# Performance work log

Measured on AMD Instinct MI355X. Metric: run time of the kernel, lower is better.

Reference implementation:

```python
import jax, jax.numpy as jnp
import numpy as np

N_NODES = 50000
N_EDGES = 800000
IN_F = 128
HID = 128
OUT = 2


def setup_inputs() -> dict:
    key = jax.random.key(0)
    ks = jax.random.split(key, 10)
    x = jax.random.normal(ks[0], (N_NODES, IN_F), dtype=jnp.float32)
    edge_index = jax.random.randint(ks[1], (2, N_EDGES), 0, N_NODES, dtype=jnp.int64)

    def lin(k, fan_in, fan_out):
        s = 1.0 / np.sqrt(fan_in)
        return jax.random.uniform(k, (fan_in, fan_out), jnp.float32, -s, s)

    return {
        "x": x,
        "edge_index": edge_index,
        # SAGEConv1: lin_l applied to mean-aggregated neighbors (with bias),
        # lin_r applied to root features (no bias), PyG convention.
        "W1_l": lin(ks[2], IN_F, HID),
        "W1_r": lin(ks[3], IN_F, HID),
        "b1": jnp.zeros((HID,), jnp.float32),
        "W2_l": lin(ks[4], HID, HID),
        "W2_r": lin(ks[5], HID, HID),
        "b2": jnp.zeros((HID,), jnp.float32),
        "Wfc": lin(ks[6], HID, OUT),
        "bfc": jnp.zeros((OUT,), jnp.float32),
    }


def reference(x, edge_index, W1_l, W1_r, b1, W2_l, W2_r, b2, Wfc, bfc):
    n = x.shape[0]
    src = edge_index[0]  # message source j
    dst = edge_index[1]  # aggregation target i
    # in-degree for mean aggregation (clamp to avoid div-by-zero for isolated nodes)
    deg = jax.ops.segment_sum(jnp.ones_like(dst, dtype=x.dtype), dst, num_segments=n)
    inv_deg = 1.0 / jnp.maximum(deg, 1.0)  # [n]

    def sage_conv(h, Wl, Wr, b):
        # mean over incoming neighbor features, then two linear maps
        agg = jax.ops.segment_sum(h[src], dst, num_segments=n) * inv_deg[:, None]
        return agg @ Wl + h @ Wr + b

    # dropout is identity at inference (training=False)
    h = jax.nn.relu(sage_conv(x, W1_l, W1_r, b1))
    h = jax.nn.relu(sage_conv(h, W2_l, W2_r, b2))
    return h @ Wfc + bfc  # [n, out] logits
```

## Files before the change

kernel.cpp:

```cpp
#include <hip/hip_runtime.h>

#define NN 50000
#define NE 800000
#define BSHIFT 9
#define NB_BUCKET ((NN + 511) >> BSHIFT)
#define BCAP 16384
#define EPB 2048
#define NBLK_E ((NE + EPB - 1) / EPB)

#define CVT_BLKS 6250
#define PREP_BLKS 32
#define SETUP_GRID (CVT_BLKS + PREP_BLKS + 1)

typedef short short8 __attribute__((ext_vector_type(8)));
typedef short short4v __attribute__((ext_vector_type(4)));
typedef float f32x4 __attribute__((ext_vector_type(4)));
typedef _Float16 half8v __attribute__((ext_vector_type(8)));

__device__ inline unsigned short f16_bits(float f) {
    _Float16 h = (_Float16)f;
    return __builtin_bit_cast(unsigned short, h);
}

__global__ __launch_bounds__(256) void setup_kernel(const float* __restrict__ x,
                                                    unsigned short* __restrict__ xb,
                                                    const float* __restrict__ W0,
                                                    const float* __restrict__ W1,
                                                    const float* __restrict__ W2,
                                                    const float* __restrict__ W3,
                                                    short* __restrict__ wf,
                                                    int* __restrict__ cursor0) {
    int b = blockIdx.x;
    if (b < CVT_BLKS) {
        int i = b * 256 + threadIdx.x;
        float4 v = ((const float4*)x)[i];
        short4v r;
        r[0] = (short)f16_bits(v.x);
        r[1] = (short)f16_bits(v.y);
        r[2] = (short)f16_bits(v.z);
        r[3] = (short)f16_bits(v.w);
        ((short4v*)xb)[i] = r;
    } else if (b < CVT_BLKS + PREP_BLKS) {
        int t = (b - CVT_BLKS) * 256 + threadIdx.x;
        int mat = t >> 11;
        const float* W = (mat == 0) ? W0 : (mat == 1) ? W1 : (mat == 2) ? W2 : W3;
        short* out = wf + (size_t)mat * 16384;
        int r = t & 2047;
        int nt = r >> 8;
        int kc = (r >> 6) & 3;
        int lane = r & 63;
        int n = nt * 16 + (lane & 15);
        int kbase = kc * 32 + ((lane >> 4) << 3);
        short8 vh;
#pragma unroll
        for (int j = 0; j < 8; ++j) {
            float w = W[(size_t)(kbase + j) * 128 + n];
            vh[j] = (short)f16_bits(w);
        }
        size_t o = ((size_t)((nt * 4 + kc) * 64 + lane)) * 8;
        *(short8*)(out + o) = vh;
    } else {
        if (threadIdx.x < NB_BUCKET) cursor0[threadIdx.x] = 0;
    }
}

__global__ __launch_bounds__(256) void binA_kernel(const int* __restrict__ src,
                                                   const int* __restrict__ dst,
                                                   int* __restrict__ cursor0,
                                                   unsigned* __restrict__ packed, int ne) {
    __shared__ int cnt[NB_BUCKET];
    __shared__ int gstart[NB_BUCKET];
    __shared__ int cur[NB_BUCKET];
    int t = threadIdx.x;
    if (t < NB_BUCKET) cnt[t] = 0;
    __syncthreads();
    int base = blockIdx.x * EPB + t * 8;
    int s[8], d[8];
    int m = 0;
    if (base + 8 <= ne) {
        *(int4*)&s[0] = *(const int4*)(src + base);
        *(int4*)&s[4] = *(const int4*)(src + base + 4);
        *(int4*)&d[0] = *(const int4*)(dst + base);
        *(int4*)&d[4] = *(const int4*)(dst + base + 4);
        m = 8;
    } else if (base < ne) {
        m = ne - base;
        for (int i = 0; i < m; ++i) { s[i] = src[base + i]; d[i] = dst[base + i]; }
    }
    for (int i = 0; i < m; ++i) atomicAdd(&cnt[d[i] >> BSHIFT], 1);
    __syncthreads();
    if (t < NB_BUCKET) {
        gstart[t] = t * BCAP + atomicAdd(&cursor0[t], cnt[t]);
        cur[t] = 0;
    }
    __syncthreads();
    for (int i = 0; i < m; ++i) {
        int b = d[i] >> BSHIFT;
        int l = atomicAdd(&cur[b], 1);
        packed[gstart[b] + l] = ((unsigned)(d[i] & 511) << 16) | (unsigned)s[i];
    }
}

__global__ __launch_bounds__(512) void binB_kernel(const unsigned* __restrict__ packed,
                                                   const int* __restrict__ cursor0,
                                                   int* __restrict__ row_ptr,
                                                   float* __restrict__ inv_deg,
                                                   int* __restrict__ col, int n, int ne) {
    __shared__ int sdeg[512];
    __shared__ int scur[512];
    __shared__ int scnt[NB_BUCKET];
    __shared__ int sebeg[NB_BUCKET];
    int b = blockIdx.x, t = threadIdx.x;
    if (t < NB_BUCKET) scnt[t] = cursor0[t];
    sdeg[t] = 0;
    __syncthreads();
    if (t == 0) {
        int run = 0;
        for (int i = 0; i < NB_BUCKET; ++i) { sebeg[i] = run; run += scnt[i]; }
    }
    __syncthreads();
    int ebeg = sebeg[b];
    int cntE = scnt[b];
    const unsigned* pk = packed + (size_t)b * BCAP;
    for (int e = t; e < cntE; e += 512) atomicAdd(&sdeg[pk[e] >> 16], 1);
    __syncthreads();
    int v = sdeg[t];
    for (int d = 1; d < 512; d <<= 1) {
        int u = (t >= d) ? sdeg[t - d] : 0;
        __syncthreads();
        sdeg[t] += u;
        __syncthreads();
    }
    int excl = sdeg[t] - v;
    scur[t] = excl;
    int node = (b << BSHIFT) + t;
    if (node < n) {
        row_ptr[node] = ebeg + excl;
        inv_deg[node] = 1.0f / (float)(v > 0 ? v : 1);
    }
    if (b == 0 && t == 0) row_ptr[n] = ne;
    __syncthreads();
    for (int e = t; e < cntE; e += 512) {
        unsigned w = pk[e];
        int dl = w >> 16;
        int pos = ebeg + atomicAdd(&scur[dl], 1);
        col[pos] = (int)(w & 0xffffu);
    }
}

__global__ __launch_bounds__(256) void fused_sage(const unsigned short* __restrict__ hb,
                                                  const int* __restrict__ row_ptr,
                                                  const int* __restrict__ col,
                                                  const float* __restrict__ inv_deg,
                                                  const short* __restrict__ Wf0,
                                                  const short* __restrict__ Wf1,
                                                  const float* __restrict__ bias,
                                                  unsigned short* __restrict__ outb,
                                                  const float* __restrict__ Wfc,
                                                  const float* __restrict__ bfc,
                                                  float* __restrict__ fcout,
                                                  int n, int relu) {
    int lane = threadIdx.x & 63;
    int wave = threadIdx.x >> 6;
    int quad = lane >> 4, m16 = lane & 15;
    int row_base = blockIdx.x * 64 + wave * 16;
    int arow = row_base + m16;
    if (arow > n - 1) arow = n - 1;

    int beg = row_ptr[arow], end = row_ptr[arow + 1];
    float accg[4][8];
#pragma unroll
    for (int kc = 0; kc < 4; ++kc)
#pragma unroll
        for (int j = 0; j < 8; ++j) accg[kc][j] = 0.f;

    const unsigned short* tq = hb + (quad << 3);
    int e = beg;
    for (; e + 4 <= end; e += 4) {
        int c0 = col[e], c1 = col[e + 1], c2 = col[e + 2], c3 = col[e + 3];
        const unsigned short* r0 = tq + ((size_t)c0 << 7);
        const unsigned short* r1 = tq + ((size_t)c1 << 7);
        const unsigned short* r2 = tq + ((size_t)c2 << 7);
        const unsigned short* r3 = tq + ((size_t)c3 << 7);
#pragma unroll
        for (int kc = 0; kc < 4; ++kc) {
            half8v v0 = *(const half8v*)(r0 + kc * 32);
            half8v v1 = *(const half8v*)(r1 + kc * 32);
            half8v v2 = *(const half8v*)(r2 + kc * 32);
            half8v v3 = *(const half8v*)(r3 + kc * 32);
#pragma unroll
            for (int j = 0; j < 8; ++j)
                accg[kc][j] += (float)v0[j] + (float)v1[j] + ((float)v2[j] + (float)v3[j]);
        }
    }
    for (; e < end; ++e) {
        const unsigned short* r0 = tq + ((size_t)col[e] << 7);
#pragma unroll
        for (int kc = 0; kc < 4; ++kc) {
            half8v v0 = *(const half8v*)(r0 + kc * 32);
#pragma unroll
            for (int j = 0; j < 8; ++j) accg[kc][j] += (float)v0[j];
        }
    }

    float sdeg = inv_deg[arow];
    half8v a0[4];
#pragma unroll
    for (int kc = 0; kc < 4; ++kc)
#pragma unroll
        for (int j = 0; j < 8; ++j) a0[kc][j] = (_Float16)(accg[kc][j] * sdeg);

    half8v a1[4];
#pragma unroll
    for (int kc = 0; kc < 4; ++kc)
        a1[kc] = *(const half8v*)(hb + ((size_t)arow << 7) + kc * 32 + (quad << 3));

    f32x4 acc[8];
#pragma unroll
    for (int nt = 0; nt < 8; ++nt) acc[nt] = (f32x4){0.f, 0.f, 0.f, 0.f};

#pragma unroll
    for (int kc = 0; kc < 4; ++kc) {
        const short* wp0 = Wf0 + ((size_t)kc * 64 + lane) * 8;
        const short* wp1 = Wf1 + ((size_t)kc * 64 + lane) * 8;
#pragma unroll
        for (int nt = 0; nt < 8; ++nt) {
            half8v b0 = *(const half8v*)(wp0 + (size_t)nt * 2048);
            half8v b1 = *(const half8v*)(wp1 + (size_t)nt * 2048);
            acc[nt] = __builtin_amdgcn_mfma_f32_16x16x32_f16(a0[kc], b0, acc[nt], 0, 0, 0);
            acc[nt] = __builtin_amdgcn_mfma_f32_16x16x32_f16(a1[kc], b1, acc[nt], 0, 0, 0);
        }
    }

    float bcol[8];
#pragma unroll
    for (int nt = 0; nt < 8; ++nt) bcol[nt] = bias[nt * 16 + m16];

    if (Wfc) {
        float w0[8], w1[8];
#pragma unroll
        for (int nt = 0; nt < 8; ++nt) {
            float2 wv = *(const float2*)(Wfc + 2 * (nt * 16 + m16));
            w0[nt] = wv.x;
            w1[nt] = wv.y;
        }
        float b0 = bfc[0], b1 = bfc[1];
#pragma unroll
        for (int r = 0; r < 4; ++r) {
            float p0 = 0.f, p1 = 0.f;
#pragma unroll
            for (int nt = 0; nt < 8; ++nt) {
                float v = fmaxf(acc[nt][r] + bcol[nt], 0.f);
                p0 += v * w0[nt];
                p1 += v * w1[nt];
            }
#pragma unroll
            for (int off = 1; off < 16; off <<= 1) {
                p0 += __shfl_xor(p0, off, 64);
                p1 += __shfl_xor(p1, off, 64);
            }
            int row = row_base + quad * 4 + r;
            if (m16 == 0 && row < n) {
                float2 o;
                o.x = p0 + b0;
                o.y = p1 + b1;
                *(float2*)(fcout + 2 * (size_t)row) = o;
            }
        }
    } else {
#pragma unroll
        for (int r = 0; r < 4; ++r) {
            int row = row_base + quad * 4 + r;
            if (row >= n) continue;
            unsigned short* opb = outb + ((size_t)row << 7) + m16;
#pragma unroll
            for (int nt = 0; nt < 8; ++nt) {
                float v = acc[nt][r] + bcol[nt];
                if (relu) v = fmaxf(v, 0.f);
                opb[nt * 16] = f16_bits(v);
            }
        }
    }
}

extern "C" void kernel_launch(void* const* d_in, const int* in_sizes, int n_in,
                              void* d_out, int out_size, void* d_ws, size_t ws_size,
                              hipStream_t stream) {
    const float* x   = (const float*)d_in[0];
    const int* edge  = (const int*)d_in[1];
    const float* W1l = (const float*)d_in[2];
    const float* W1r = (const float*)d_in[3];
    const float* b1  = (const float*)d_in[4];
    const float* W2l = (const float*)d_in[5];
    const float* W2r = (const float*)d_in[6];
    const float* b2  = (const float*)d_in[7];
    const float* Wfc = (const float*)d_in[8];
    const float* bfc = (const float*)d_in[9];
    float* out = (float*)d_out;

    const int n = NN, ne = NE;
    const int* src = edge;
    const int* dst = edge + ne;

    char* ws = (char*)d_ws;
    size_t off = 0;
    auto alloc = [&](size_t bytes) -> char* {
        char* p = ws + off;
        off = (off + bytes + 511) & ~(size_t)511;
        return p;
    };
    int* row_ptr     = (int*)alloc((size_t)(n + 1) * 4);
    float* invdeg    = (float*)alloc((size_t)n * 4);
    int* cursor0     = (int*)alloc((size_t)NB_BUCKET * 4);
    short* wf        = (short*)alloc((size_t)4 * 16384 * 2);
    unsigned* packed = (unsigned*)alloc((size_t)NB_BUCKET * BCAP * 4);
    int* col         = (int*)alloc((size_t)ne * 4);
    unsigned short* xb   = (unsigned short*)alloc((size_t)n * 128 * 2);
    unsigned short* h1b  = (unsigned short*)alloc((size_t)n * 128 * 2);
    (void)ws_size; (void)in_sizes; (void)n_in; (void)out_size;

    setup_kernel<<<SETUP_GRID, 256, 0, stream>>>(x, xb, W1l, W1r, W2l, W2r, wf, cursor0);
    binA_kernel<<<NBLK_E, 256, 0, stream>>>(src, dst, cursor0, packed, ne);
    binB_kernel<<<NB_BUCKET, 512, 0, stream>>>(packed, cursor0, row_ptr, invdeg, col, n, ne);

    fused_sage<<<(n + 63) / 64, 256, 0, stream>>>(xb, row_ptr, col, invdeg,
                                                  wf, wf + 16384, b1, h1b,
                                                  (const float*)0, (const float*)0, (float*)0, n, 1);
    fused_sage<<<(n + 63) / 64, 256, 0, stream>>>(h1b, row_ptr, col, invdeg,
                                                  wf + 2 * 16384, wf + 3 * 16384, b2,
                                                  (unsigned short*)0, Wfc, bfc, out, n, 1);
}
```

Before: 230.5 us.

## Split neighbor gather across two waves per tile and reduce partials via LDS

Doubles the block to 512 threads so each 16-row tile gets two waves, each gathering half of every row's neighbor list, with the partial sums combined through shared memory before the MFMA stage. The gather loop is unrolled to 8 edges and sums neighbors in fp16 vector adds before converting to fp32, which cuts conversion work but loses some accumulation precision. It targets latency in the memory-bound gather by raising memory-level parallelism, at the cost of 32KB of LDS per block, a block-wide barrier, and idle upper-half waves during the matmul.

```diff
diff --git a/kernel.cpp b/kernel.cpp
--- a/kernel.cpp
+++ b/kernel.cpp
@@ -148,7 +148,7 @@
     }
 }
 
-__global__ __launch_bounds__(256) void fused_sage(const unsigned short* __restrict__ hb,
+__global__ __launch_bounds__(512) void fused_sage(const unsigned short* __restrict__ hb,
                                                   const int* __restrict__ row_ptr,
                                                   const int* __restrict__ col,
                                                   const float* __restrict__ inv_deg,
@@ -160,14 +160,28 @@
                                                   const float* __restrict__ bfc,
                                                   float* __restrict__ fcout,
                                                   int n, int relu) {
+    __shared__ float plds[32 * 256];
     int lane = threadIdx.x & 63;
-    int wave = threadIdx.x >> 6;
+    int wv = threadIdx.x >> 6;
+    int tile = wv & 3;
+    int half = wv >> 2;
     int quad = lane >> 4, m16 = lane & 15;
-    int row_base = blockIdx.x * 64 + wave * 16;
+    int row_base = blockIdx.x * 64 + tile * 16;
     int arow = row_base + m16;
     if (arow > n - 1) arow = n - 1;
 
     int beg = row_ptr[arow], end = row_ptr[arow + 1];
+    int mid = beg + ((end - beg) >> 1);
+    int gb = half ? mid : beg;
+    int ge = half ? end : mid;
+
+    half8v a1[4];
+    if (!half) {
+#pragma unroll
+        for (int kc = 0; kc < 4; ++kc)
+            a1[kc] = *(const half8v*)(hb + ((size_t)arow << 7) + kc * 32 + (quad << 3));
+    }
+
     float accg[4][8];
 #pragma unroll
     for (int kc = 0; kc < 4; ++kc)
@@ -175,33 +189,61 @@
         for (int j = 0; j < 8; ++j) accg[kc][j] = 0.f;
 
     const unsigned short* tq = hb + (quad << 3);
-    int e = beg;
-    for (; e + 4 <= end; e += 4) {
-        int c0 = col[e], c1 = col[e + 1], c2 = col[e + 2], c3 = col[e + 3];
-        const unsigned short* r0 = tq + ((size_t)c0 << 7);
-        const unsigned short* r1 = tq + ((size_t)c1 << 7);
-        const unsigned short* r2 = tq + ((size_t)c2 << 7);
-        const unsigned short* r3 = tq + ((size_t)c3 << 7);
+    int e = gb;
+    for (; e + 8 <= ge; e += 8) {
+        const unsigned short* rp[8];
+#pragma unroll
+        for (int j = 0; j < 8; ++j) rp[j] = tq + ((size_t)col[e + j] << 7);
+#pragma unroll
+        for (int kc = 0; kc < 4; ++kc) {
+            half8v v[8];
+#pragma unroll
+            for (int j = 0; j < 8; ++j) v[j] = *(const half8v*)(rp[j] + kc * 32);
+            half8v s = ((v[0] + v[1]) + (v[2] + v[3])) + ((v[4] + v[5]) + (v[6] + v[7]));
+#pragma unroll
+            for (int q = 0; q < 8; ++q) accg[kc][q] += (float)s[q];
+        }
+    }
+    if (e + 4 <= ge) {
+        const unsigned short* rp[4];
+#pragma unroll
+        for (int j = 0; j < 4; ++j) rp[j] = tq + ((size_t)col[e + j] << 7);
+#pragma unroll
+        for (int kc = 0; kc < 4; ++kc) {
+            half8v v[4];
+#pragma unroll
+            for (int j = 0; j < 4; ++j) v[j] = *(const half8v*)(rp[j] + kc * 32);
+            half8v s = (v[0] + v[1]) + (v[2] + v[3]);
+#pragma unroll
+            for (int q = 0; q < 8; ++q) accg[kc][q] += (float)s[q];
+        }
+        e += 4;
+    }
+    for (; e < ge; ++e) {
+        const unsigned short* r0 = tq + ((size_t)col[e] << 7);
 #pragma unroll
         for (int kc = 0; kc < 4; ++kc) {
             half8v v0 = *(const half8v*)(r0 + kc * 32);
-            half8v v1 = *(const half8v*)(r1 + kc * 32);
-            half8v v2 = *(const half8v*)(r2 + kc * 32);
-            half8v v3 = *(const half8v*)(r3 + kc * 32);
+#pragma unroll
+            for (int q = 0; q < 8; ++q) accg[kc][q] += (float)v0[q];
+        }
+    }
+
+    int slot = tile * 64 + lane;
+    if (half) {
+#pragma unroll
+        for (int kc = 0; kc < 4; ++kc)
 #pragma unroll
             for (int j = 0; j < 8; ++j)
-                accg[kc][j] += (float)v0[j] + (float)v1[j] + ((float)v2[j] + (float)v3[j]);
-        }
-    }
-    for (; e < end; ++e) {
-        const unsigned short* r0 = tq + ((size_t)col[e] << 7);
-#pragma unroll
-        for (int kc = 0; kc < 4; ++kc) {
-            half8v v0 = *(const half8v*)(r0 + kc * 32);
-#pragma unroll
-            for (int j = 0; j < 8; ++j) accg[kc][j] += (float)v0[j];
-        }
-    }
+                plds[(kc * 8 + j) * 256 + slot] = accg[kc][j];
+    }
+    __syncthreads();
+    if (half) return;
+#pragma unroll
+    for (int kc = 0; kc < 4; ++kc)
+#pragma unroll
+        for (int j = 0; j < 8; ++j)
+            accg[kc][j] += plds[(kc * 8 + j) * 256 + slot];
 
     float sdeg = inv_deg[arow];
     half8v a0[4];
@@ -209,11 +251,6 @@
     for (int kc = 0; kc < 4; ++kc)
 #pragma unroll
         for (int j = 0; j < 8; ++j) a0[kc][j] = (_Float16)(accg[kc][j] * sdeg);
-
-    half8v a1[4];
-#pragma unroll
-    for (int kc = 0; kc < 4; ++kc)
-        a1[kc] = *(const half8v*)(hb + ((size_t)arow << 7) + kc * 32 + (quad << 3));
 
     f32x4 acc[8];
 #pragma unroll
@@ -240,9 +277,9 @@
         float w0[8], w1[8];
 #pragma unroll
         for (int nt = 0; nt < 8; ++nt) {
-            float2 wv = *(const float2*)(Wfc + 2 * (nt * 16 + m16));
-            w0[nt] = wv.x;
-            w1[nt] = wv.y;
+            float2 wv2 = *(const float2*)(Wfc + 2 * (nt * 16 + m16));
+            w0[nt] = wv2.x;
+            w1[nt] = wv2.y;
         }
         float b0 = bfc[0], b1 = bfc[1];
 #pragma unroll
@@ -323,10 +360,10 @@
     binA_kernel<<<NBLK_E, 256, 0, stream>>>(src, dst, cursor0, packed, ne);
     binB_kernel<<<NB_BUCKET, 512, 0, stream>>>(packed, cursor0, row_ptr, invdeg, col, n, ne);
 
-    fused_sage<<<(n + 63) / 64, 256, 0, stream>>>(xb, row_ptr, col, invdeg,
+    fused_sage<<<(n + 63) / 64, 512, 0, stream>>>(xb, row_ptr, col, invdeg,
                                                   wf, wf + 16384, b1, h1b,
                                                   (const float*)0, (const float*)0, (float*)0, n, 1);
-    fused_sage<<<(n + 63) / 64, 256, 0, stream>>>(h1b, row_ptr, col, invdeg,
+    fused_sage<<<(n + 63) / 64, 512, 0, stream>>>(h1b, row_ptr, col, invdeg,
                                                   wf + 2 * 16384, wf + 3 * 16384, b2,
                                                   (unsigned short*)0, Wfc, bfc, out, n, 1);
 }
```

Result: slower. 245.0 us (+6.3%).
